# Kernel optimization log

Measured on AMD Instinct MI355X. Metric: run time of the kernel, lower is better.

The kernel has to match this reference:

```python
import jax, jax.numpy as jnp
import numpy as np

N_USERS = 100000
N_ITEMS = 100000
EMB = 64
N_NODES = N_USERS + N_ITEMS + 2  # +1 padding row each for users and items
N_EDGES = 1200000
N_BEHAVIORS = 3
LAYERS = [3, 3, 3]
EPS = 1e-12  # F.normalize eps


def setup_inputs() -> dict:
    key = jax.random.key(0)
    k1, k2, k3, k4, k5 = jax.random.split(key, 5)
    user_emb = jax.random.normal(k1, (N_USERS + 1, EMB), dtype=jnp.float32)
    item_emb = jax.random.normal(k2, (N_ITEMS + 1, EMB), dtype=jnp.float32)
    rows = jax.random.randint(k3, (N_BEHAVIORS, N_EDGES), 0, N_NODES, dtype=jnp.int32)
    cols = jax.random.randint(k4, (N_BEHAVIORS, N_EDGES), 0, N_NODES, dtype=jnp.int32)
    weights = jax.random.uniform(k5, (N_BEHAVIORS, N_EDGES), dtype=jnp.float32)
    return {"user_emb": user_emb, "item_emb": item_emb, "rows": rows,
            "cols": cols, "weights": weights}


def _spmm(rows_b, cols_b, w_b, x):
    # sparse [N,N] @ dense [N,D] via gather + segment-sum (COO SpMM)
    msg = x[cols_b] * w_b[:, None]                      # [E, D]
    return jax.ops.segment_sum(msg, rows_b, num_segments=N_NODES)


def _l2_normalize(x):
    norm = jnp.sqrt(jnp.sum(x * x, axis=-1, keepdims=True))
    return x / jnp.maximum(norm, EPS)


def reference(user_emb, item_emb, rows, cols, weights):
    # NSED.gcn_propagate: sequential LightGCN per behavior with residual chaining
    total = jnp.concatenate([user_emb, item_emb], axis=0)  # [N, D]
    outs = []
    for b in range(N_BEHAVIORS):
        x = total
        acc = x            # running sum of layer embeddings (== mean of stack)
        for _ in range(LAYERS[b]):
            x = _spmm(rows[b], cols[b], weights[b], x)
            acc = acc + x
        lightgcn_emb = acc / jnp.float32(LAYERS[b] + 1)    # stack+mean over layers
        total = _l2_normalize(lightgcn_emb) + total
        outs.append(total)
    return jnp.stack(outs, axis=0)  # [B, N, D]
```

## Files before the change

### kernel.cpp

```cpp
#include <hip/hip_runtime.h>
#include <math.h>

#define N_USERS 100000
#define N_ITEMS 100000
#define EMB 64
#define N_NODES (N_USERS + N_ITEMS + 2)
#define N_EDGES 1200000
#define E3 (3 * N_EDGES)
#define N3 (3 * N_NODES)
#define ND ((long)N_NODES * (long)EMB)

#define BUCKET_BITS 9
#define KPB 512
#define NBUCKET ((N3 + KPB - 1) / KPB)
#define CAP 3584
#define EPB 4096
#define NB_P1 ((E3 + EPB - 1) / EPB)

typedef float f32x4 __attribute__((ext_vector_type(4)));
typedef float f32x8 __attribute__((ext_vector_type(8)));
typedef unsigned short u16x4 __attribute__((ext_vector_type(4)));
typedef unsigned short u16x8 __attribute__((ext_vector_type(8)));

__device__ inline unsigned short f2bf(float f) {
    unsigned int u = __float_as_uint(f);
    return (unsigned short)((u + 0x7FFFu + ((u >> 16) & 1u)) >> 16);
}

__device__ inline void fma8(f32x8& acc, float w, u16x8 s) {
    #pragma unroll
    for (int j = 0; j < 8; ++j)
        acc[j] = fmaf(w, __uint_as_float((unsigned int)s[j] << 16), acc[j]);
}
__device__ inline f32x8 bf8_to_f8(u16x8 s) {
    f32x8 f;
    #pragma unroll
    for (int j = 0; j < 8; ++j) f[j] = __uint_as_float((unsigned int)s[j] << 16);
    return f;
}
__device__ inline u16x8 f8_to_bf8(f32x8 f) {
    u16x8 s;
    #pragma unroll
    for (int j = 0; j < 8; ++j) s[j] = f2bf(f[j]);
    return s;
}

__global__ void concat_kernel(const float4* __restrict__ u,
                              const float4* __restrict__ it,
                              float4* __restrict__ t,
                              u16x4* __restrict__ tb) {
    long i = (long)blockIdx.x * blockDim.x + threadIdx.x;
    if (i >= ND / 4) return;
    long n = i >> 4;
    float4 v = (n < (long)(N_USERS + 1)) ? u[i] : it[i - (long)(N_USERS + 1) * 16];
    t[i] = v;
    u16x4 b;
    b.x = f2bf(v.x); b.y = f2bf(v.y); b.z = f2bf(v.z); b.w = f2bf(v.w);
    tb[i] = b;
}

__global__ void init_bcur_kernel(int* __restrict__ bcur) {
    int i = blockIdx.x * blockDim.x + threadIdx.x;
    if (i < NBUCKET) bcur[i] = i * CAP;
}

__global__ void bucket_scatter_kernel(const int* __restrict__ rows,
                                      const int* __restrict__ cols,
                                      const float* __restrict__ w,
                                      int* __restrict__ bcur,
                                      int2* __restrict__ tmpedge) {
    __shared__ int h[NBUCKET];
    __shared__ int lbase[NBUCKET];
    for (int i = threadIdx.x; i < NBUCKET; i += 512) h[i] = 0;
    __syncthreads();
    long base = (long)blockIdx.x * EPB;
    int keys[EPB / 512];
    for (int k = 0; k < EPB / 512; ++k) {
        long e = base + k * 512 + threadIdx.x;
        int key = -1;
        if (e < E3) {
            int b = (e >= 2L * N_EDGES) ? 2 : ((e >= N_EDGES) ? 1 : 0);
            key = b * N_NODES + rows[e];
            atomicAdd(&h[key >> BUCKET_BITS], 1);
        }
        keys[k] = key;
    }
    __syncthreads();
    for (int i = threadIdx.x; i < NBUCKET; i += 512) {
        int c = h[i];
        lbase[i] = c ? atomicAdd(&bcur[i], c) : 0;
        h[i] = 0;
    }
    __syncthreads();
    for (int k = 0; k < EPB / 512; ++k) {
        long e = base + k * 512 + threadIdx.x;
        int key = keys[k];
        if (key >= 0) {
            int bk = key >> BUCKET_BITS;
            int pos = lbase[bk] + atomicAdd(&h[bk], 1);
            int2 pk;
            pk.x = ((key & (KPB - 1)) << 18) | cols[e];
            pk.y = __float_as_int(w[e]);
            tmpedge[pos] = pk;
        }
    }
}

__global__ void bucket_scan_kernel(const int* __restrict__ bcur, int* __restrict__ bbase,
                                   int* __restrict__ rowptr) {
    __shared__ int sm[1024];
    __shared__ int carry;
    int tid = threadIdx.x;
    if (tid == 0) carry = 0;
    __syncthreads();
    for (int base = 0; base < NBUCKET; base += 1024) {
        int i = base + tid;
        int v = (i < NBUCKET) ? (bcur[i] - i * CAP) : 0;
        sm[tid] = v;
        __syncthreads();
        for (int off = 1; off < 1024; off <<= 1) {
            int t = (tid >= off) ? sm[tid - off] : 0;
            __syncthreads();
            sm[tid] += t;
            __syncthreads();
        }
        if (i < NBUCKET) bbase[i] = sm[tid] - v + carry;
        __syncthreads();
        if (tid == 0) carry += sm[1023];
        __syncthreads();
    }
    if (tid == 0) { bbase[NBUCKET] = E3; rowptr[N3] = E3; }
}

__global__ void bucket_sort_kernel(const int* __restrict__ bbase,
                                   const int2* __restrict__ tmpedge,
                                   int2* __restrict__ sedge,
                                   int* __restrict__ rowptr) {
    int g = blockIdx.x;
    int s = bbase[g];
    int cnt = bbase[g + 1] - s;
    long tb = (long)g * CAP;
    __shared__ int h[KPB];
    __shared__ int ex[KPB];
    __shared__ int tmp[256];
    int tid = threadIdx.x;
    h[tid * 2] = 0; h[tid * 2 + 1] = 0;
    __syncthreads();
    for (int i = tid; i < cnt; i += 256) atomicAdd(&h[tmpedge[tb + i].x >> 18], 1);
    __syncthreads();
    int a0 = h[tid * 2], a1 = h[tid * 2 + 1];
    int psum = a0 + a1;
    tmp[tid] = psum;
    __syncthreads();
    for (int off = 1; off < 256; off <<= 1) {
        int t = (tid >= off) ? tmp[tid - off] : 0;
        __syncthreads();
        tmp[tid] += t;
        __syncthreads();
    }
    int pex = tmp[tid] - psum;
    ex[tid * 2] = pex;
    ex[tid * 2 + 1] = pex + a0;
    __syncthreads();
    for (int j = tid; j < KPB; j += 256) {
        int key = g * KPB + j;
        if (key < N3) rowptr[key] = s + ex[j];
    }
    h[tid * 2] = ex[tid * 2];
    h[tid * 2 + 1] = ex[tid * 2 + 1];
    __syncthreads();
    for (int i = tid; i < cnt; i += 256) {
        int2 pk = tmpedge[tb + i];
        int kl = pk.x >> 18;
        int pos = s + atomicAdd(&h[kl], 1);
        int2 o;
        o.x = pk.x & 0x3FFFF;
        o.y = pk.y;
        sedge[pos] = o;
    }
}

__global__ void spmm_bf16_kernel(const int* __restrict__ rowptr,
                                 const int2* __restrict__ sedge,
                                 const u16x8* __restrict__ x,
                                 u16x8* __restrict__ y) {
    int wid  = threadIdx.x >> 6;
    int lane = threadIdx.x & 63;
    int r = lane >> 3;
    int q = lane & 7;
    int n = (blockIdx.x * 4 + wid) * 8 + r;
    if (n >= N_NODES) return;
    int s = rowptr[n], e = rowptr[n + 1];
    f32x8 acc = {0.f, 0.f, 0.f, 0.f, 0.f, 0.f, 0.f, 0.f};
    int i = s;
    for (; i + 4 <= e; i += 4) {
        int2 e0 = sedge[i], e1 = sedge[i + 1], e2 = sedge[i + 2], e3 = sedge[i + 3];
        u16x8 b0 = x[(long)e0.x * 8 + q];
        u16x8 b1 = x[(long)e1.x * 8 + q];
        u16x8 b2 = x[(long)e2.x * 8 + q];
        u16x8 b3 = x[(long)e3.x * 8 + q];
        fma8(acc, __int_as_float(e0.y), b0);
        fma8(acc, __int_as_float(e1.y), b1);
        fma8(acc, __int_as_float(e2.y), b2);
        fma8(acc, __int_as_float(e3.y), b3);
    }
    if (i + 2 <= e) {
        int2 e0 = sedge[i], e1 = sedge[i + 1];
        u16x8 b0 = x[(long)e0.x * 8 + q];
        u16x8 b1 = x[(long)e1.x * 8 + q];
        fma8(acc, __int_as_float(e0.y), b0);
        fma8(acc, __int_as_float(e1.y), b1);
        i += 2;
    }
    if (i < e) {
        int2 e0 = sedge[i];
        u16x8 b0 = x[(long)e0.x * 8 + q];
        fma8(acc, __int_as_float(e0.y), b0);
    }
    __builtin_nontemporal_store(f8_to_bf8(acc), &y[(long)n * 8 + q]);
}

__global__ void spmm_final_kernel(const int* __restrict__ rowptr,
                                  const int2* __restrict__ sedge,
                                  const u16x8* __restrict__ Qb,
                                  const float* __restrict__ Tin,
                                  const u16x8* __restrict__ Pb,
                                  float* __restrict__ outp,
                                  u16x8* __restrict__ TbOut) {
    int wid  = threadIdx.x >> 6;
    int lane = threadIdx.x & 63;
    int r = lane >> 3;
    int q = lane & 7;
    int n = (blockIdx.x * 4 + wid) * 8 + r;
    if (n >= N_NODES) return;
    int s = rowptr[n], e = rowptr[n + 1];
    f32x8 acc = {0.f, 0.f, 0.f, 0.f, 0.f, 0.f, 0.f, 0.f};
    int i = s;
    for (; i + 4 <= e; i += 4) {
        int2 e0 = sedge[i], e1 = sedge[i + 1], e2 = sedge[i + 2], e3 = sedge[i + 3];
        u16x8 b0 = Qb[(long)e0.x * 8 + q];
        u16x8 b1 = Qb[(long)e1.x * 8 + q];
        u16x8 b2 = Qb[(long)e2.x * 8 + q];
        u16x8 b3 = Qb[(long)e3.x * 8 + q];
        fma8(acc, __int_as_float(e0.y), b0);
        fma8(acc, __int_as_float(e1.y), b1);
        fma8(acc, __int_as_float(e2.y), b2);
        fma8(acc, __int_as_float(e3.y), b3);
    }
    if (i + 2 <= e) {
        int2 e0 = sedge[i], e1 = sedge[i + 1];
        u16x8 b0 = Qb[(long)e0.x * 8 + q];
        u16x8 b1 = Qb[(long)e1.x * 8 + q];
        fma8(acc, __int_as_float(e0.y), b0);
        fma8(acc, __int_as_float(e1.y), b1);
        i += 2;
    }
    if (i < e) {
        int2 e0 = sedge[i];
        u16x8 b0 = Qb[(long)e0.x * 8 + q];
        fma8(acc, __int_as_float(e0.y), b0);
    }
    long o = (long)n * 8 + q;
    f32x8 t = *(const f32x8*)(Tin + (long)n * EMB + q * 8);
    f32x8 p = bf8_to_f8(Pb[o]);
    f32x8 qv = bf8_to_f8(Qb[o]);
    f32x8 v;
    float ss = 0.f;
    #pragma unroll
    for (int j = 0; j < 8; ++j) {
        v[j] = (t[j] + p[j] + qv[j] + acc[j]) * 0.25f;
        ss = fmaf(v[j], v[j], ss);
    }
    ss += __shfl_xor(ss, 1, 64);
    ss += __shfl_xor(ss, 2, 64);
    ss += __shfl_xor(ss, 4, 64);
    float inv = 1.0f / fmaxf(sqrtf(ss), 1e-12f);
    f32x8 ov;
    #pragma unroll
    for (int j = 0; j < 8; ++j) ov[j] = fmaf(v[j], inv, t[j]);
    __builtin_nontemporal_store(ov, (f32x8*)(outp + (long)n * EMB + q * 8));
    if (TbOut) __builtin_nontemporal_store(f8_to_bf8(ov), &TbOut[o]);
}

extern "C" void kernel_launch(void* const* d_in, const int* in_sizes, int n_in,
                              void* d_out, int out_size, void* d_ws, size_t ws_size,
                              hipStream_t stream) {
    const float* user_emb = (const float*)d_in[0];
    const float* item_emb = (const float*)d_in[1];
    const int*   rows     = (const int*)d_in[2];
    const int*   cols     = (const int*)d_in[3];
    const float* weights  = (const float*)d_in[4];
    float* out = (float*)d_out;

    unsigned short* Tb   = (unsigned short*)d_ws;
    unsigned short* Pq   = Tb + ND;
    unsigned short* Qq   = Pq + ND;
    int2* tmpedge = (int2*)(Qq + ND);
    int2* sedge   = tmpedge + (long)NBUCKET * CAP;
    int*  rowptr  = (int*)(sedge + E3);
    int*  bbase   = rowptr + N3 + 2;
    int*  bcur    = bbase + NBUCKET + 2;

    float* o0 = out;
    float* o1 = out + ND;
    float* o2 = out + 2 * ND;
    float* T0 = o2;

    const long v4_blocks  = (ND / 4 + 255) / 256;
    const long row_blocks = ((long)N_NODES + 31) / 32;

    init_bcur_kernel<<<(NBUCKET + 255) / 256, 256, 0, stream>>>(bcur);
    bucket_scatter_kernel<<<NB_P1, 512, 0, stream>>>(rows, cols, weights, bcur, tmpedge);
    bucket_scan_kernel<<<1, 1024, 0, stream>>>(bcur, bbase, rowptr);
    bucket_sort_kernel<<<NBUCKET, 256, 0, stream>>>(bbase, tmpedge, sedge, rowptr);

    concat_kernel<<<v4_blocks, 256, 0, stream>>>((const float4*)user_emb,
                                                 (const float4*)item_emb,
                                                 (float4*)T0, (u16x4*)Tb);

    float* Tins[3] = { T0, o0, o1 };
    float* Dsts[3] = { o0, o1, o2 };

    for (int b = 0; b < 3; ++b) {
        const int* rp = rowptr + (long)b * N_NODES;
        u16x8* Pb = (u16x8*)Pq;
        u16x8* Qb = (u16x8*)Qq;

        spmm_bf16_kernel<<<row_blocks, 256, 0, stream>>>(rp, sedge, (const u16x8*)Tb, Pb);
        spmm_bf16_kernel<<<row_blocks, 256, 0, stream>>>(rp, sedge, (const u16x8*)Pb, Qb);
        spmm_final_kernel<<<row_blocks, 256, 0, stream>>>(rp, sedge, (const u16x8*)Qb,
                                                          Tins[b], (const u16x8*)Pb,
                                                          Dsts[b],
                                                          (b < 2) ? (u16x8*)Tb : nullptr);
    }
}
```

Baseline: 466.6 us.

## Enlarge sort buckets, unroll SpMM gathers by 8, drop fp32 concat copy

Doubles keys per bucket and threads per block in the scatter and sort stages, reducing the number of sort blocks. Unrolls the SpMM edge loop to issue eight independent gathers at once, for more memory-level parallelism. Removes the fp32 concatenated copy of the input embeddings; the first final kernel reads directly from the user/item arrays. Bucket capacity margin is tighter relative to the mean bucket load, and the larger unroll raises register pressure.

```diff
diff --git a/kernel.cpp b/kernel.cpp
--- a/kernel.cpp
+++ b/kernel.cpp
@@ -10,11 +10,11 @@
 #define N3 (3 * N_NODES)
 #define ND ((long)N_NODES * (long)EMB)
 
-#define BUCKET_BITS 9
-#define KPB 512
+#define KPB 1024
 #define NBUCKET ((N3 + KPB - 1) / KPB)
-#define CAP 3584
-#define EPB 4096
+#define CAP 6656
+#define EPB 8192
+#define SCT 512
 #define NB_P1 ((E3 + EPB - 1) / EPB)
 
 typedef float f32x4 __attribute__((ext_vector_type(4)));
@@ -26,7 +26,6 @@
     unsigned int u = __float_as_uint(f);
     return (unsigned short)((u + 0x7FFFu + ((u >> 16) & 1u)) >> 16);
 }
-
 __device__ inline void fma8(f32x8& acc, float w, u16x8 s) {
     #pragma unroll
     for (int j = 0; j < 8; ++j)
@@ -45,15 +44,13 @@
     return s;
 }
 
-__global__ void concat_kernel(const float4* __restrict__ u,
-                              const float4* __restrict__ it,
-                              float4* __restrict__ t,
-                              u16x4* __restrict__ tb) {
+__global__ void make_tb_kernel(const float4* __restrict__ u,
+                               const float4* __restrict__ it,
+                               u16x4* __restrict__ tb) {
     long i = (long)blockIdx.x * blockDim.x + threadIdx.x;
     if (i >= ND / 4) return;
     long n = i >> 4;
     float4 v = (n < (long)(N_USERS + 1)) ? u[i] : it[i - (long)(N_USERS + 1) * 16];
-    t[i] = v;
     u16x4 b;
     b.x = f2bf(v.x); b.y = f2bf(v.y); b.z = f2bf(v.z); b.w = f2bf(v.w);
     tb[i] = b;
@@ -71,32 +68,32 @@
                                       int2* __restrict__ tmpedge) {
     __shared__ int h[NBUCKET];
     __shared__ int lbase[NBUCKET];
-    for (int i = threadIdx.x; i < NBUCKET; i += 512) h[i] = 0;
+    for (int i = threadIdx.x; i < NBUCKET; i += SCT) h[i] = 0;
     __syncthreads();
     long base = (long)blockIdx.x * EPB;
-    int keys[EPB / 512];
-    for (int k = 0; k < EPB / 512; ++k) {
-        long e = base + k * 512 + threadIdx.x;
+    int keys[EPB / SCT];
+    for (int k = 0; k < EPB / SCT; ++k) {
+        long e = base + k * SCT + threadIdx.x;
         int key = -1;
         if (e < E3) {
             int b = (e >= 2L * N_EDGES) ? 2 : ((e >= N_EDGES) ? 1 : 0);
             key = b * N_NODES + rows[e];
-            atomicAdd(&h[key >> BUCKET_BITS], 1);
+            atomicAdd(&h[key / KPB], 1);
         }
         keys[k] = key;
     }
     __syncthreads();
-    for (int i = threadIdx.x; i < NBUCKET; i += 512) {
+    for (int i = threadIdx.x; i < NBUCKET; i += SCT) {
         int c = h[i];
         lbase[i] = c ? atomicAdd(&bcur[i], c) : 0;
         h[i] = 0;
     }
     __syncthreads();
-    for (int k = 0; k < EPB / 512; ++k) {
-        long e = base + k * 512 + threadIdx.x;
+    for (int k = 0; k < EPB / SCT; ++k) {
+        long e = base + k * SCT + threadIdx.x;
         int key = keys[k];
         if (key >= 0) {
-            int bk = key >> BUCKET_BITS;
+            int bk = key / KPB;
             int pos = lbase[bk] + atomicAdd(&h[bk], 1);
             int2 pk;
             pk.x = ((key & (KPB - 1)) << 18) | cols[e];
@@ -142,17 +139,17 @@
     long tb = (long)g * CAP;
     __shared__ int h[KPB];
     __shared__ int ex[KPB];
-    __shared__ int tmp[256];
+    __shared__ int tmp[512];
     int tid = threadIdx.x;
     h[tid * 2] = 0; h[tid * 2 + 1] = 0;
     __syncthreads();
-    for (int i = tid; i < cnt; i += 256) atomicAdd(&h[tmpedge[tb + i].x >> 18], 1);
+    for (int i = tid; i < cnt; i += 512) atomicAdd(&h[tmpedge[tb + i].x >> 18], 1);
     __syncthreads();
     int a0 = h[tid * 2], a1 = h[tid * 2 + 1];
     int psum = a0 + a1;
     tmp[tid] = psum;
     __syncthreads();
-    for (int off = 1; off < 256; off <<= 1) {
+    for (int off = 1; off < 512; off <<= 1) {
         int t = (tid >= off) ? tmp[tid - off] : 0;
         __syncthreads();
         tmp[tid] += t;
@@ -162,14 +159,14 @@
     ex[tid * 2] = pex;
     ex[tid * 2 + 1] = pex + a0;
     __syncthreads();
-    for (int j = tid; j < KPB; j += 256) {
+    for (int j = tid; j < KPB; j += 512) {
         int key = g * KPB + j;
         if (key < N3) rowptr[key] = s + ex[j];
     }
     h[tid * 2] = ex[tid * 2];
     h[tid * 2 + 1] = ex[tid * 2 + 1];
     __syncthreads();
-    for (int i = tid; i < cnt; i += 256) {
+    for (int i = tid; i < cnt; i += 512) {
         int2 pk = tmpedge[tb + i];
         int kl = pk.x >> 18;
         int pos = s + atomicAdd(&h[kl], 1);
@@ -193,7 +190,17 @@
     int s = rowptr[n], e = rowptr[n + 1];
     f32x8 acc = {0.f, 0.f, 0.f, 0.f, 0.f, 0.f, 0.f, 0.f};
     int i = s;
-    for (; i + 4 <= e; i += 4) {
+    for (; i + 8 <= e; i += 8) {
+        int2 ee[8];
+        u16x8 bb[8];
+        #pragma unroll
+        for (int j = 0; j < 8; ++j) ee[j] = sedge[i + j];
+        #pragma unroll
+        for (int j = 0; j < 8; ++j) bb[j] = x[(long)ee[j].x * 8 + q];
+        #pragma unroll
+        for (int j = 0; j < 8; ++j) fma8(acc, __int_as_float(ee[j].y), bb[j]);
+    }
+    if (i + 4 <= e) {
         int2 e0 = sedge[i], e1 = sedge[i + 1], e2 = sedge[i + 2], e3 = sedge[i + 3];
         u16x8 b0 = x[(long)e0.x * 8 + q];
         u16x8 b1 = x[(long)e1.x * 8 + q];
@@ -203,6 +210,7 @@
         fma8(acc, __int_as_float(e1.y), b1);
         fma8(acc, __int_as_float(e2.y), b2);
         fma8(acc, __int_as_float(e3.y), b3);
+        i += 4;
     }
     if (i + 2 <= e) {
         int2 e0 = sedge[i], e1 = sedge[i + 1];
@@ -224,6 +232,8 @@
                                   const int2* __restrict__ sedge,
                                   const u16x8* __restrict__ Qb,
                                   const float* __restrict__ Tin,
+                                  const float* __restrict__ uemb,
+                                  const float* __restrict__ iemb,
                                   const u16x8* __restrict__ Pb,
                                   float* __restrict__ outp,
                                   u16x8* __restrict__ TbOut) {
@@ -236,7 +246,17 @@
     int s = rowptr[n], e = rowptr[n + 1];
     f32x8 acc = {0.f, 0.f, 0.f, 0.f, 0.f, 0.f, 0.f, 0.f};
     int i = s;
-    for (; i + 4 <= e; i += 4) {
+    for (; i + 8 <= e; i += 8) {
+        int2 ee[8];
+        u16x8 bb[8];
+        #pragma unroll
+        for (int j = 0; j < 8; ++j) ee[j] = sedge[i + j];
+        #pragma unroll
+        for (int j = 0; j < 8; ++j) bb[j] = Qb[(long)ee[j].x * 8 + q];
+        #pragma unroll
+        for (int j = 0; j < 8; ++j) fma8(acc, __int_as_float(ee[j].y), bb[j]);
+    }
+    if (i + 4 <= e) {
         int2 e0 = sedge[i], e1 = sedge[i + 1], e2 = sedge[i + 2], e3 = sedge[i + 3];
         u16x8 b0 = Qb[(long)e0.x * 8 + q];
         u16x8 b1 = Qb[(long)e1.x * 8 + q];
@@ -246,6 +266,7 @@
         fma8(acc, __int_as_float(e1.y), b1);
         fma8(acc, __int_as_float(e2.y), b2);
         fma8(acc, __int_as_float(e3.y), b3);
+        i += 4;
     }
     if (i + 2 <= e) {
         int2 e0 = sedge[i], e1 = sedge[i + 1];
@@ -260,8 +281,12 @@
         u16x8 b0 = Qb[(long)e0.x * 8 + q];
         fma8(acc, __int_as_float(e0.y), b0);
     }
+    const float* tsrc;
+    if (Tin) tsrc = Tin + (long)n * EMB;
+    else if (n <= N_USERS) tsrc = uemb + (long)n * EMB;
+    else tsrc = iemb + (long)(n - N_USERS - 1) * EMB;
     long o = (long)n * 8 + q;
-    f32x8 t = *(const f32x8*)(Tin + (long)n * EMB + q * 8);
+    f32x8 t = *(const f32x8*)(tsrc + q * 8);
     f32x8 p = bf8_to_f8(Pb[o]);
     f32x8 qv = bf8_to_f8(Qb[o]);
     f32x8 v;
@@ -304,22 +329,20 @@
     float* o0 = out;
     float* o1 = out + ND;
     float* o2 = out + 2 * ND;
-    float* T0 = o2;
 
     const long v4_blocks  = (ND / 4 + 255) / 256;
     const long row_blocks = ((long)N_NODES + 31) / 32;
 
     init_bcur_kernel<<<(NBUCKET + 255) / 256, 256, 0, stream>>>(bcur);
-    bucket_scatter_kernel<<<NB_P1, 512, 0, stream>>>(rows, cols, weights, bcur, tmpedge);
+    bucket_scatter_kernel<<<NB_P1, SCT, 0, stream>>>(rows, cols, weights, bcur, tmpedge);
     bucket_scan_kernel<<<1, 1024, 0, stream>>>(bcur, bbase, rowptr);
-    bucket_sort_kernel<<<NBUCKET, 256, 0, stream>>>(bbase, tmpedge, sedge, rowptr);
-
-    concat_kernel<<<v4_blocks, 256, 0, stream>>>((const float4*)user_emb,
-                                                 (const float4*)item_emb,
-                                                 (float4*)T0, (u16x4*)Tb);
-
-    float* Tins[3] = { T0, o0, o1 };
-    float* Dsts[3] = { o0, o1, o2 };
+    bucket_sort_kernel<<<NBUCKET, 512, 0, stream>>>(bbase, tmpedge, sedge, rowptr);
+
+    make_tb_kernel<<<v4_blocks, 256, 0, stream>>>((const float4*)user_emb,
+                                                  (const float4*)item_emb, (u16x4*)Tb);
+
+    const float* Tins[3] = { nullptr, o0, o1 };
+    float*       Dsts[3] = { o0, o1, o2 };
 
     for (int b = 0; b < 3; ++b) {
         const int* rp = rowptr + (long)b * N_NODES;
@@ -329,8 +352,8 @@
         spmm_bf16_kernel<<<row_blocks, 256, 0, stream>>>(rp, sedge, (const u16x8*)Tb, Pb);
         spmm_bf16_kernel<<<row_blocks, 256, 0, stream>>>(rp, sedge, (const u16x8*)Pb, Qb);
         spmm_final_kernel<<<row_blocks, 256, 0, stream>>>(rp, sedge, (const u16x8*)Qb,
-                                                          Tins[b], (const u16x8*)Pb,
-                                                          Dsts[b],
+                                                          Tins[b], user_emb, item_emb,
+                                                          (const u16x8*)Pb, Dsts[b],
                                                           (b < 2) ? (u16x8*)Tb : nullptr);
     }
 }
```

Measured after the change: 470.1 us. About the same (+0.7%).
